# Kernel tuning notes

Measured on AMD Instinct MI355X. Metric: run time of the kernel, lower is better.

The kernel has to match this reference:

```python
import jax, jax.numpy as jnp
import numpy as np

HEADS = 8
REL_MAX = 64  # module-level constant REL_MAX_DIST


def _to_c(x):
    # x: [..., 2] real/imag interleaved (torch.view_as_real layout) -> complex
    return jax.lax.complex(x[..., 0], x[..., 1])


def setup_inputs() -> dict:
    key = jax.random.key(0)
    ks = jax.random.split(key, 12)
    dim, past_len = 256, 65536
    d2 = dim * 2
    s = 1.0 / np.sqrt(d2)  # torch Linear default init range

    def lin(k):
        kw, kb = jax.random.split(k)
        W = jax.random.uniform(kw, (d2, d2), jnp.float32, -s, s)
        b = jax.random.uniform(kb, (d2,), jnp.float32, -s, s)
        return W, b

    Wq, bq = lin(ks[0])
    Wk, bk = lin(ks[1])
    Wv, bv = lin(ks[2])
    Wo, bo = lin(ks[3])
    return {
        "curr_pos": past_len,
        "z_curr": jax.random.normal(ks[4], (dim, 2), jnp.float32),
        "z_past": jax.random.normal(ks[5], (past_len, dim, 2), jnp.float32),
        "Wq": Wq, "bq": bq, "Wk": Wk, "bk": bk,
        "Wv": Wv, "bv": bv, "Wo": Wo, "bo": bo,
        "rel_bias": jax.random.normal(ks[6], (2 * REL_MAX + 1, dim, 2), jnp.float32) * 0.02,
    }


def reference(curr_pos, z_curr, z_past, Wq, bq, Wk, bk, Wv, bv, Wo, bo, rel_bias):
    dim = z_curr.shape[0]
    past_len = z_past.shape[0]
    head_dim = dim // HEADS

    # real-valued linear projections on interleaved (real, imag) features
    q_proj = z_curr.reshape(-1) @ Wq.T + bq                        # [2*dim]
    k_proj = z_past.reshape(past_len, -1) @ Wk.T + bk              # [L, 2*dim]
    v_proj = z_past.reshape(past_len, -1) @ Wv.T + bv              # [L, 2*dim]

    # view as complex, split heads
    q_h = _to_c(q_proj.reshape(dim, 2)).reshape(HEADS, head_dim)               # [H, hd]
    k_h = _to_c(k_proj.reshape(past_len, dim, 2)).reshape(past_len, HEADS, head_dim)
    v_h = _to_c(v_proj.reshape(past_len, dim, 2)).reshape(past_len, HEADS, head_dim)

    # Re(<q, k>) per head
    dot_scores = jnp.real(jnp.conj(q_h)[None] * k_h).sum(-1)       # [L, H]

    # relative positional bias (gather + clamp)
    rel_dists = jnp.arange(curr_pos - past_len, curr_pos)
    idx = jnp.clip(rel_dists + REL_MAX, 0, 2 * REL_MAX)
    rb_h = _to_c(rel_bias)[idx].reshape(past_len, HEADS, head_dim)
    rel_scores = jnp.real(jnp.conj(q_h)[None] * rb_h).sum(-1)      # [L, H]

    scores = (dot_scores + rel_scores) / np.sqrt(head_dim)
    weights = jax.nn.softmax(scores, axis=0)                       # softmax over past_len

    out_h = (weights[..., None] * v_h).sum(0)                      # [H, hd] complex
    out_c = out_h.reshape(dim)
    out_real = jnp.stack([jnp.real(out_c), jnp.imag(out_c)], -1).reshape(-1)  # [2*dim]
    out = out_real @ Wo.T + bo
    # return real view [dim, 2] of the complex output (view_as_complex layout)
    return out.reshape(dim, 2)
```

## Files before the change

### kernel.cpp

```cpp
#include <hip/hip_runtime.h>
#include <math.h>


static constexpr float SCALE = 0.17677669529663687f;

__device__ __forceinline__ float wave_sum(float v) {
#pragma unroll
  for (int off = 32; off > 0; off >>= 1) v += __shfl_xor(v, off, 64);
  return v;
}

__global__ __launch_bounds__(256) void k_matvec512(
    const float* __restrict__ M, const float* __restrict__ x,
    const float* __restrict__ bias, float* __restrict__ y) {
  const int wave = threadIdx.x >> 6, lane = threadIdx.x & 63;
  const int j = blockIdx.x * 4 + wave;
  const float* Mr = M + (size_t)j * 512 + lane * 8;
  const float4 m0 = *(const float4*)Mr;
  const float4 m1 = *(const float4*)(Mr + 4);
  const float4 x0 = *(const float4*)(x + lane * 8);
  const float4 x1 = *(const float4*)(x + lane * 8 + 4);
  float acc = m0.x * x0.x + m0.y * x0.y + m0.z * x0.z + m0.w * x0.w +
              m1.x * x1.x + m1.y * x1.y + m1.z * x1.z + m1.w * x1.w;
  acc = wave_sum(acc);
  if (lane == 0) y[j] = acc + bias[j];
}

__global__ __launch_bounds__(256) void k_front2(
    const float* __restrict__ Wk, const float* __restrict__ qp,
    const float* __restrict__ bk, const float* __restrict__ rb,
    float* __restrict__ wk, float* __restrict__ ck, float* __restrict__ relq,
    float* __restrict__ S_un, float* __restrict__ s) {
  __shared__ float ql[512];
  const int b = blockIdx.x;
  if (b < 16) {
    const int h = b >> 1;
    if (threadIdx.x < 64) ql[threadIdx.x] = qp[h * 64 + threadIdx.x];
    __syncthreads();
    const int i = (b & 1) * 256 + threadIdx.x;
    float acc = 0.f;
#pragma unroll
    for (int k = 0; k < 64; ++k)
      acc += ql[k] * Wk[(size_t)(h * 64 + k) * 512 + i];
    wk[h * 512 + i] = acc * SCALE;
  } else if (b < 22) {
    for (int t = threadIdx.x; t < 512; t += 256) ql[t] = qp[t];
    __syncthreads();
    const int t = (b - 16) * 256 + threadIdx.x;
    if (t < 129 * 8) {
      const int idx = t >> 3, h = t & 7;
      float acc = 0.f;
#pragma unroll
      for (int k = 0; k < 64; ++k)
        acc += ql[h * 64 + k] * rb[(size_t)idx * 512 + h * 64 + k];
      relq[t] = acc * SCALE;
    }
  } else if (b == 22) {
    if (threadIdx.x < 8) {
      const int h = threadIdx.x;
      float acc = 0.f;
      for (int k = 0; k < 64; ++k) acc += qp[h * 64 + k] * bk[h * 64 + k];
      ck[h] = acc * SCALE;
    }
  } else {
    for (int t = threadIdx.x; t < 4096; t += 256) S_un[t] = 0.f;
    if (threadIdx.x < 8) s[threadIdx.x] = 0.f;
  }
}

__global__ __launch_bounds__(256, 2) void k_attn(
    const float* __restrict__ zp, const float* __restrict__ wk,
    const float* __restrict__ ck, const float* __restrict__ relq,
    const int* __restrict__ curr_pos, int L, float* __restrict__ S_un,
    float* __restrict__ s_out) {
  __shared__ float relql[1032];
  __shared__ float Sl[4096];
  __shared__ float sl[4][8];
  const int tid = threadIdx.x;
  const int wave = tid >> 6, lane = tid & 63;
  for (int t = tid; t < 1032; t += 256) relql[t] = relq[t];

  float wkr[8][8];
#pragma unroll
  for (int h = 0; h < 8; ++h) {
    const float4 a = *(const float4*)(wk + h * 512 + lane * 8);
    const float4 b = *(const float4*)(wk + h * 512 + lane * 8 + 4);
    wkr[h][0] = a.x; wkr[h][1] = a.y; wkr[h][2] = a.z; wkr[h][3] = a.w;
    wkr[h][4] = b.x; wkr[h][5] = b.y; wkr[h][6] = b.z; wkr[h][7] = b.w;
  }
  const int myh = ((lane & 1) << 2) | (lane & 2) | ((lane >> 2) & 1);
  const float ck_my = ck[myh];
  const int cp = curr_pos[0];
  __syncthreads();

  float S[8][8];
#pragma unroll
  for (int h = 0; h < 8; ++h)
#pragma unroll
    for (int k = 0; k < 8; ++k) S[h][k] = 0.f;
  float s_loc = 0.f;

  const int l0 = blockIdx.x * 128 + wave * 32;
  const float* zr = zp + (size_t)l0 * 512 + lane * 8;
  float4 p0 = *(const float4*)zr;
  float4 p1 = *(const float4*)(zr + 4);
  const float* z1p = (l0 + 1 < L) ? (zr + 512) : zr;
  float4 q0 = *(const float4*)z1p;
  float4 q1 = *(const float4*)(z1p + 4);

#pragma unroll 2
  for (int r = 0; r < 32; ++r) {
    const int l = l0 + r;
    const float* zn = (l + 2 < L) ? (zr + 1024) : zr;
    const float4 n0 = *(const float4*)zn;
    const float4 n1 = *(const float4*)(zn + 4);
    const float zz[8] = {p0.x, p0.y, p0.z, p0.w, p1.x, p1.y, p1.z, p1.w};
    float acc[8];
#pragma unroll
    for (int h = 0; h < 8; ++h) {
      float a = 0.f;
#pragma unroll
      for (int k = 0; k < 8; ++k) a += zz[k] * wkr[h][k];
      acc[h] = a;
    }
    const bool lo1 = (lane & 1) == 0;
    float b0 = (lo1 ? acc[0] : acc[4]) + __shfl_xor(lo1 ? acc[4] : acc[0], 1, 64);
    float b1 = (lo1 ? acc[1] : acc[5]) + __shfl_xor(lo1 ? acc[5] : acc[1], 1, 64);
    float b2 = (lo1 ? acc[2] : acc[6]) + __shfl_xor(lo1 ? acc[6] : acc[2], 1, 64);
    float b3 = (lo1 ? acc[3] : acc[7]) + __shfl_xor(lo1 ? acc[7] : acc[3], 1, 64);
    const bool lo2 = (lane & 2) == 0;
    float c0 = (lo2 ? b0 : b2) + __shfl_xor(lo2 ? b2 : b0, 2, 64);
    float c1 = (lo2 ? b1 : b3) + __shfl_xor(lo2 ? b3 : b1, 2, 64);
    const bool lo3 = (lane & 4) == 0;
    float d = (lo3 ? c0 : c1) + __shfl_xor(lo3 ? c1 : c0, 4, 64);
    d += __shfl_xor(d, 8, 64);
    d += __shfl_xor(d, 16, 64);
    d += __shfl_xor(d, 32, 64);

    int dd = cp - L + l + 64;
    dd = dd < 0 ? 0 : (dd > 128 ? 128 : dd);
    float w = __expf(d + ck_my + relql[dd * 8 + myh]);
    if (l >= L) w = 0.f;
    s_loc += w;
#pragma unroll
    for (int h = 0; h < 8; ++h) {
      const int src = ((h & 1) << 2) | (h & 2) | ((h >> 2) & 1);
      const float wh = __shfl(w, src, 64);
#pragma unroll
      for (int k = 0; k < 8; ++k) S[h][k] += wh * zz[k];
    }
    p0 = q0; p1 = q1; q0 = n0; q1 = n1; zr += 512;
  }

  if (lane < 8) sl[wave][myh] = s_loc;
  for (int wv = 0; wv < 4; ++wv) {
    if (wave == wv) {
#pragma unroll
      for (int h = 0; h < 8; ++h)
#pragma unroll
        for (int k = 0; k < 8; ++k) {
          const int idx = h * 512 + lane * 8 + k;
          if (wv == 0) Sl[idx] = S[h][k];
          else Sl[idx] += S[h][k];
        }
    }
    __syncthreads();
  }
  for (int t = tid; t < 4096; t += 256) atomicAdd(&S_un[t], Sl[t]);
  if (tid < 8)
    atomicAdd(&s_out[tid], sl[0][tid] + sl[1][tid] + sl[2][tid] + sl[3][tid]);
}

__global__ __launch_bounds__(256) void k_outreal(
    const float* __restrict__ Wv, const float* __restrict__ S_un,
    const float* __restrict__ s, const float* __restrict__ bv,
    float* __restrict__ out_real) {
  const int wave = threadIdx.x >> 6, lane = threadIdx.x & 63;
  const int j = blockIdx.x * 4 + wave;
  const int h = j >> 6;
  const float* Mr = Wv + (size_t)j * 512 + lane * 8;
  const float* xr = S_un + h * 512 + lane * 8;
  const float4 m0 = *(const float4*)Mr;
  const float4 m1 = *(const float4*)(Mr + 4);
  const float4 x0 = *(const float4*)xr;
  const float4 x1 = *(const float4*)(xr + 4);
  float acc = m0.x * x0.x + m0.y * x0.y + m0.z * x0.z + m0.w * x0.w +
              m1.x * x1.x + m1.y * x1.y + m1.z * x1.z + m1.w * x1.w;
  acc = wave_sum(acc);
  if (lane == 0) out_real[j] = acc / s[h] + bv[j];
}

extern "C" void kernel_launch(void* const* d_in, const int* in_sizes, int n_in,
                              void* d_out, int out_size, void* d_ws,
                              size_t ws_size, hipStream_t stream) {
  const int* curr_pos = (const int*)d_in[0];
  const float* z_curr = (const float*)d_in[1];
  const float* z_past = (const float*)d_in[2];
  const float* Wq = (const float*)d_in[3];
  const float* bq = (const float*)d_in[4];
  const float* Wk = (const float*)d_in[5];
  const float* bk = (const float*)d_in[6];
  const float* Wv = (const float*)d_in[7];
  const float* bv = (const float*)d_in[8];
  const float* Wo = (const float*)d_in[9];
  const float* bo = (const float*)d_in[10];
  const float* rb = (const float*)d_in[11];
  float* out = (float*)d_out;

  const int L = in_sizes[2] / 512;
  const int nb = (L + 127) / 128;

  float* ws = (float*)d_ws;
  size_t o = 0;
  float* qp = ws + o;       o += 512;
  float* wkb = ws + o;      o += 8 * 512;
  float* ckb = ws + o;      o += 16;
  float* relq = ws + o;     o += 1040;
  float* sb = ws + o;       o += 8;
  float* S_un = ws + o;     o += 4096;
  float* out_real = ws + o; o += 512;
  (void)ws_size; (void)n_in; (void)out_size;

  k_matvec512<<<128, 256, 0, stream>>>(Wq, z_curr, bq, qp);
  k_front2<<<24, 256, 0, stream>>>(Wk, qp, bk, rb, wkb, ckb, relq, S_un, sb);
  k_attn<<<nb, 256, 0, stream>>>(z_past, wkb, ckb, relq, curr_pos, L, S_un, sb);
  k_outreal<<<128, 256, 0, stream>>>(Wv, S_un, sb, bv, out_real);
  k_matvec512<<<128, 256, 0, stream>>>(Wo, out_real, bo, out);
}
```

Baseline: 260.4 us.

## Replace global atomic accumulation with per-block partials and separate reduction kernel

Each attention block now writes its 4096-entry weighted sum and its 8 softmax denominators to a per-block partial buffer instead of atomically adding into one global accumulator. A new combine kernel reduces the partials in 16 groups per column, with a few atomics per column, and has one block sum the denominators. This targets contention from 512 blocks each issuing 4096 atomics to the same addresses. In exchange it adds a kernel launch and about 8 MB of extra global writes and reads for the partials.

```diff
diff --git a/kernel.cpp b/kernel.cpp
--- a/kernel.cpp
+++ b/kernel.cpp
@@ -30,7 +30,7 @@
     const float* __restrict__ Wk, const float* __restrict__ qp,
     const float* __restrict__ bk, const float* __restrict__ rb,
     float* __restrict__ wk, float* __restrict__ ck, float* __restrict__ relq,
-    float* __restrict__ S_un, float* __restrict__ s) {
+    float* __restrict__ S_un) {
   __shared__ float ql[512];
   const int b = blockIdx.x;
   if (b < 16) {
@@ -64,15 +64,14 @@
     }
   } else {
     for (int t = threadIdx.x; t < 4096; t += 256) S_un[t] = 0.f;
-    if (threadIdx.x < 8) s[threadIdx.x] = 0.f;
   }
 }
 
 __global__ __launch_bounds__(256, 2) void k_attn(
     const float* __restrict__ zp, const float* __restrict__ wk,
     const float* __restrict__ ck, const float* __restrict__ relq,
-    const int* __restrict__ curr_pos, int L, float* __restrict__ S_un,
-    float* __restrict__ s_out) {
+    const int* __restrict__ curr_pos, int L, float* __restrict__ Sp,
+    float* __restrict__ sp) {
   __shared__ float relql[1032];
   __shared__ float Sl[4096];
   __shared__ float sl[4][8];
@@ -166,9 +165,47 @@
     }
     __syncthreads();
   }
-  for (int t = tid; t < 4096; t += 256) atomicAdd(&S_un[t], Sl[t]);
+  for (int t = tid; t < 4096; t += 256)
+    Sp[(size_t)blockIdx.x * 4096 + t] = Sl[t];
   if (tid < 8)
-    atomicAdd(&s_out[tid], sl[0][tid] + sl[1][tid] + sl[2][tid] + sl[3][tid]);
+    sp[blockIdx.x * 8 + tid] = sl[0][tid] + sl[1][tid] + sl[2][tid] + sl[3][tid];
+}
+
+__global__ __launch_bounds__(256) void k_comb2(
+    const float* __restrict__ Sp, const float* __restrict__ spv, int nb,
+    float* __restrict__ S_un, float* __restrict__ s) {
+  if (blockIdx.x < 256) {
+    const int T = blockIdx.x * 256 + threadIdx.x;
+    const int col = T & 4095;
+    const int g = T >> 12;
+    const int chunk = (nb + 15) >> 4;
+    const int r0 = g * chunk;
+    const int r1 = min(r0 + chunk, nb);
+    float a[8];
+#pragma unroll
+    for (int u = 0; u < 8; ++u) a[u] = 0.f;
+    int b = r0;
+    for (; b + 8 <= r1; b += 8) {
+#pragma unroll
+      for (int u = 0; u < 8; ++u) a[u] += Sp[(size_t)(b + u) * 4096 + col];
+    }
+    for (; b < r1; ++b) a[0] += Sp[(size_t)b * 4096 + col];
+    const float t = ((a[0] + a[1]) + (a[2] + a[3])) +
+                    ((a[4] + a[5]) + (a[6] + a[7]));
+    atomicAdd(&S_un[col], t);
+  } else {
+    __shared__ float red[256];
+    float a = 0.f;
+    for (int b2 = threadIdx.x >> 3; b2 < nb; b2 += 32)
+      a += spv[b2 * 8 + (threadIdx.x & 7)];
+    red[threadIdx.x] = a;
+    __syncthreads();
+    if (threadIdx.x < 8) {
+      float x = 0.f;
+      for (int c = 0; c < 32; ++c) x += red[c * 8 + threadIdx.x];
+      s[threadIdx.x] = x;
+    }
+  }
 }
 
 __global__ __launch_bounds__(256) void k_outreal(
@@ -217,13 +254,16 @@
   float* ckb = ws + o;      o += 16;
   float* relq = ws + o;     o += 1040;
   float* sb = ws + o;       o += 8;
+  float* sp = ws + o;       o += (size_t)nb * 8;
   float* S_un = ws + o;     o += 4096;
   float* out_real = ws + o; o += 512;
+  float* Sp = ws + o;       o += (size_t)nb * 4096;
   (void)ws_size; (void)n_in; (void)out_size;
 
   k_matvec512<<<128, 256, 0, stream>>>(Wq, z_curr, bq, qp);
-  k_front2<<<24, 256, 0, stream>>>(Wk, qp, bk, rb, wkb, ckb, relq, S_un, sb);
-  k_attn<<<nb, 256, 0, stream>>>(z_past, wkb, ckb, relq, curr_pos, L, S_un, sb);
+  k_front2<<<24, 256, 0, stream>>>(Wk, qp, bk, rb, wkb, ckb, relq, S_un);
+  k_attn<<<nb, 256, 0, stream>>>(z_past, wkb, ckb, relq, curr_pos, L, Sp, sp);
+  k_comb2<<<257, 256, 0, stream>>>(Sp, sp, nb, S_un, sb);
   k_outreal<<<128, 256, 0, stream>>>(Wv, S_un, sb, bv, out_real);
   k_matvec512<<<128, 256, 0, stream>>>(Wo, out_real, bo, out);
 }
```

After: 256.5 us. No clear change (-1.5%).
